# Kernel optimization log

Hardware: AMD Instinct MI355X
Metric: run time of the kernel (lower is better)

## Reference

```python
import jax, jax.numpy as jnp
import numpy as np

# --- static config (matches init_kwargs) ---
N = 10000          # nodes
E = 160000         # edges
MULT = 16          # multiplicity (in and out)
NL = 2             # number of irreps (lvals = [0, 1])
DIM = 4            # 1 + 3 spherical dims
EDGE_DIM = 32
HID = 128
RANK = 8           # low-rank radial weight rank
H = 4              # attention heads
HM = MULT // H     # head multiplicity
IDX = np.array([0, 1, 1, 1])  # irrep index for each of the DIM positions


def _radial(ef, w1, bb1, wl, bl, wr, br):
    """Low-rank radial weight: (E, edge_dim) -> (E, NL*MULT, NL*MULT)."""
    h = jax.nn.gelu(ef @ w1 + bb1, approximate=False)
    left = (h @ wl + bl).reshape(-1, NL * MULT, RANK)
    right = (h @ wr + br).reshape(-1, RANK, NL * MULT)
    return left @ right


def _conv(b1, b2, ef, f, src, w1, bb1, wl, bl, wr, br):
    """Equivariant convolution: gather -> basis contract -> radial bmm -> basis."""
    rw = _radial(ef, w1, bb1, wl, bl, wr, br)          # (E, 2*MULT, 2*MULT)
    f_src = f[src]                                      # (E, MULT, DIM)
    t = jnp.einsum('emd,edl->eml', f_src, b1)           # (E, MULT, NL)
    t = t.reshape(E, MULT * NL)                         # row-major, matches torch view
    t = jnp.einsum('erc,ec->er', rw, t)                 # (E, NL*MULT)
    t = t.reshape(E, MULT, NL)                          # (E, out_mult, nl2)
    return jnp.einsum('eml,eld->emd', t, b2)            # (E, MULT, DIM)


def reference(b1, b2, edge_feats, f, src_idx, dst_idx,
              q_w, q_b,
              k_w1, k_b1, k_wl, k_bl, k_wr, k_br,
              v_w1, v_b1, v_wl, v_bl, v_wr, v_br):
    # --- Q: equivariant linear on node features (per-irrep weights) ---
    W = q_w.reshape(NL, MULT, MULT)[IDX]                # (DIM, out_mult, in_mult)
    q = jnp.einsum('dom,nmd->nod', W, f)                # (N, MULT, DIM)
    q = q.at[:, :, 0].add(q_b[:, 0])                    # bias on scalar (l=0) slot

    # --- K, V: equivariant convolutions over edges ---
    k = _conv(b1, b2, edge_feats, f, src_idx, k_w1, k_b1, k_wl, k_bl, k_wr, k_br)
    v = _conv(b1, b2, edge_feats, f, src_idx, v_w1, v_b1, v_wl, v_bl, v_wr, v_br)

    # --- multi-head node_wise attention scores ---
    qh = q.reshape(N, H, HM * DIM)
    kh = k.reshape(E, H, HM * DIM)
    scale = jnp.sqrt(jnp.asarray(HM * DIM, q.dtype))
    scores = jnp.sum(qh[dst_idx] * kh, axis=-1) / scale  # (E, H)

    # --- segment softmax over edges grouped by destination node ---
    m = jax.ops.segment_max(scores, dst_idx, num_segments=N)       # (N, H)
    ex = jnp.exp(scores - m[dst_idx])
    den = jax.ops.segment_sum(ex, dst_idx, num_segments=N)         # (N, H)
    alpha = ex / jnp.maximum(den[dst_idx], 1e-9)                   # (E, H)

    # --- weighted scatter-reduce of values ---
    vh = v.reshape(E, H, HM * DIM)
    out = jax.ops.segment_sum(alpha[..., None] * vh, dst_idx, num_segments=N)
    return out.reshape(N, MULT, DIM)


def setup_inputs() -> dict:
    key = jax.random.key(0)
    ks = jax.random.split(key, 24)
    s = 0.05
    inp = {
        'b1': jax.random.normal(ks[0], (E, DIM, NL), jnp.float32),
        'b2': jax.random.normal(ks[1], (E, NL, DIM), jnp.float32),
        'edge_feats': jax.random.normal(ks[2], (E, EDGE_DIM), jnp.float32),
        'f': jax.random.normal(ks[3], (N, MULT, DIM), jnp.float32),
        'src_idx': jax.random.randint(ks[4], (E,), 0, N),
        'dst_idx': jax.random.randint(ks[5], (E,), 0, N),
        # Q equivariant linear
        'q_w': jax.random.normal(ks[6], (NL * MULT, MULT), jnp.float32) * s,
        'q_b': jnp.zeros((MULT, 1), jnp.float32),
    }
    for i, p in enumerate(['k', 'v']):
        base = 8 + i * 6
        inp[p + '_w1'] = jax.random.normal(ks[base + 0], (EDGE_DIM, HID), jnp.float32) * s
        inp[p + '_b1'] = jnp.zeros((HID,), jnp.float32)
        inp[p + '_wl'] = jax.random.normal(ks[base + 2], (HID, NL * MULT * RANK), jnp.float32) * s
        inp[p + '_bl'] = jnp.zeros((NL * MULT * RANK,), jnp.float32)
        inp[p + '_wr'] = jax.random.normal(ks[base + 4], (HID, RANK * NL * MULT), jnp.float32) * s
        inp[p + '_br'] = jnp.zeros((RANK * NL * MULT,), jnp.float32)
    return inp
```

## Files before the change

kernel.cpp:

```cpp
#include <hip/hip_runtime.h>
#include <hip/hip_bf16.h>
#include <math.h>

#define NNODES 10000
#define NEDGE  160000

typedef unsigned short u16;
using bf16x8 = __attribute__((ext_vector_type(8))) short;
using u16x8  = __attribute__((ext_vector_type(8))) unsigned short;
using f32x4  = __attribute__((ext_vector_type(4))) float;

static __device__ __forceinline__ u16 f2bf(float x) {
  unsigned u = __float_as_uint(x);
  u += 0x7FFFu + ((u >> 16) & 1u);
  return (u16)(u >> 16);
}
static __device__ __forceinline__ float bf2f(u16 h) {
  return __uint_as_float(((unsigned)h) << 16);
}
static __device__ __forceinline__ unsigned pack_bf16(float a, float b) {
  __hip_bfloat162 h = __float22bfloat162_rn(make_float2(a, b));
  return *(unsigned*)&h;
}
static __device__ __forceinline__ float fast_gelu(float x) {
  float y = x * __builtin_fmaf(0.07135481283f, x * x, 1.5957691216f);
  float e = __expf(y);
  return x - x * __builtin_amdgcn_rcpf(e + 1.0f);
}

__global__ void __launch_bounds__(1024) csr_build_kernel(
    const int* __restrict__ dst, int* __restrict__ rowptr, int* __restrict__ cursor) {
  __shared__ int hist[NNODES];
  __shared__ int part[1024];
  int t = threadIdx.x;
  for (int i = t; i < NNODES; i += 1024) hist[i] = 0;
  __syncthreads();
  const int4* d4 = (const int4*)dst;
  for (int i = t; i < NEDGE / 4; i += 1024) {
    int4 v = d4[i];
    atomicAdd(&hist[v.x], 1);
    atomicAdd(&hist[v.y], 1);
    atomicAdd(&hist[v.z], 1);
    atomicAdd(&hist[v.w], 1);
  }
  __syncthreads();
  int base = t * 10;
  int local[10];
  int s = 0;
#pragma unroll
  for (int i = 0; i < 10; ++i) {
    int idx = base + i;
    local[i] = (idx < NNODES) ? hist[idx] : 0;
    s += local[i];
  }
  part[t] = s;
  __syncthreads();
  for (int o = 1; o < 1024; o <<= 1) {
    int v = (t >= o) ? part[t - o] : 0;
    __syncthreads();
    part[t] += v;
    __syncthreads();
  }
  int run = (t == 0) ? 0 : part[t - 1];
#pragma unroll
  for (int i = 0; i < 10; ++i) {
    int idx = base + i;
    if (idx < NNODES) { rowptr[idx] = run; cursor[idx] = run; run += local[i]; }
  }
  if (t == 1023) rowptr[NNODES] = run;
}

__global__ void __launch_bounds__(256) setup_kernel(
    const float* __restrict__ kwr, const float* __restrict__ kwl,
    const float* __restrict__ vwr, const float* __restrict__ vwl,
    u16* __restrict__ Wsw,
    const float* __restrict__ kw1, const float* __restrict__ vw1,
    u16* __restrict__ W1sw,
    const float* __restrict__ f, const float* __restrict__ qw,
    const float* __restrict__ qb, float* __restrict__ q) {
  int b = blockIdx.x, tid = threadIdx.x;
  if (b < 512) {
    int idx = b * 256 + tid;
    int slot = idx >> 15;
    int w = idx & 32767;
    int j = w & 7, lane = (w >> 3) & 63, ks = (w >> 9) & 3, tg = w >> 11;
    int k   = ks * 32 + ((lane >> 4) << 3) + j;
    int col = (tg << 4) + (lane & 15);
    const float* s = (slot == 0) ? kwr : (slot == 1) ? kwl : (slot == 2) ? vwr : vwl;
    Wsw[idx] = f2bf(s[k * 256 + col]);
  } else if (b < 544) {
    int idx = (b - 512) * 256 + tid;
    int slot = idx >> 12;
    int w = idx & 4095;
    int j = w & 7, lane = (w >> 3) & 63, nt = w >> 9;
    int k   = ((lane >> 4) << 3) + j;
    int col = (nt << 4) + (lane & 15);
    const float* s = (slot == 0) ? kw1 : vw1;
    W1sw[idx] = f2bf(s[k * 128 + col]);
  } else {
    int i = (b - 544) * 256 + tid;
    if (i >= NNODES * 16) return;
    int n = i >> 4, o = i & 15;
    const float* frow = f + (size_t)n * 64;
    float o0 = 0.f, o1 = 0.f, o2 = 0.f, o3 = 0.f;
#pragma unroll
    for (int m = 0; m < 16; ++m) {
      float w0 = qw[o * 16 + m];
      float w1 = qw[(16 + o) * 16 + m];
      o0 += w0 * frow[m * 4 + 0];
      o1 += w1 * frow[m * 4 + 1];
      o2 += w1 * frow[m * 4 + 2];
      o3 += w1 * frow[m * 4 + 3];
    }
    o0 += qb[o];
    float4 r = make_float4(o0, o1, o2, o3);
    *(float4*)(q + (size_t)i * 4) = r;
  }
}

__global__ void __launch_bounds__(256) fill_t_kernel(
    const int* __restrict__ dst, const int* __restrict__ src,
    const float* __restrict__ f, const float* __restrict__ b1,
    const float* __restrict__ b2, const float* __restrict__ ef,
    int* __restrict__ cursor, char* __restrict__ comb) {
  int e = blockIdx.x * 256 + threadIdx.x;
  int n = dst[e];
  int pos = atomicAdd(&cursor[n], 1);
  char* rb = comb + (size_t)pos * 192;
  const float* frow = f + (size_t)src[e] * 64;
  const float* be = b1 + (size_t)e * 8;
  float b[8];
#pragma unroll
  for (int k = 0; k < 8; ++k) b[k] = be[k];
  uint4* tp = (uint4*)rb;
#pragma unroll
  for (int mh = 0; mh < 4; ++mh) {
    unsigned pk[4];
#pragma unroll
    for (int mi = 0; mi < 4; ++mi) {
      int m = mh * 4 + mi;
      float f0 = frow[m * 4 + 0], f1 = frow[m * 4 + 1], f2 = frow[m * 4 + 2], f3 = frow[m * 4 + 3];
      float t0 = f0 * b[0] + f1 * b[2] + f2 * b[4] + f3 * b[6];
      float t1 = f0 * b[1] + f1 * b[3] + f2 * b[5] + f3 * b[7];
      pk[mi] = pack_bf16(t0, t1);
    }
    tp[mh] = make_uint4(pk[0], pk[1], pk[2], pk[3]);
  }
  const float* efe = ef + (size_t)e * 32;
#pragma unroll
  for (int g = 0; g < 4; ++g) {
    float4 v0 = *(const float4*)&efe[g * 8];
    float4 v1 = *(const float4*)&efe[g * 8 + 4];
    tp[4 + g] = make_uint4(pack_bf16(v0.x, v0.y), pack_bf16(v0.z, v0.w),
                           pack_bf16(v1.x, v1.y), pack_bf16(v1.z, v1.w));
  }
  const float* b2e = b2 + (size_t)e * 8;
  *(float4*)(rb + 128) = *(const float4*)&b2e[0];
  *(float4*)(rb + 144) = *(const float4*)&b2e[4];
  *(int*)(rb + 160) = n;
}

__global__ void __launch_bounds__(512) conv_fused_kernel(
    const char* __restrict__ comb,
    const u16* __restrict__ w1sw_k, const float* __restrict__ b1h_k,
    const u16* __restrict__ wswr_k, const float* __restrict__ br_k,
    const u16* __restrict__ wswl_k, const float* __restrict__ bl_k,
    const u16* __restrict__ w1sw_v, const float* __restrict__ b1h_v,
    const u16* __restrict__ wswr_v, const float* __restrict__ br_v,
    const u16* __restrict__ wswl_v, const float* __restrict__ bl_v,
    const float* __restrict__ qbuf, float* __restrict__ exs,
    u16* __restrict__ kv) {
  __shared__ alignas(16) u16 sA[64 * 136];
  __shared__ alignas(16) u16 t_s[64 * 40];
  __shared__ alignas(16) float b2_s[64 * 12];
  __shared__ alignas(16) float u_s[64 * 12];
  __shared__ alignas(16) float t2_pool[64 * 36];
  float* t2_s = t2_pool;
  u16*   efs  = (u16*)t2_pool;

  int tid = threadIdx.x;
  int wave = tid >> 6, lane = tid & 63, quad = lane >> 4, l16 = lane & 15;
  bool kmode = (blockIdx.x & 1) == 0;
  size_t i0 = (size_t)(blockIdx.x >> 1) * 64;

  const u16*   w1sw = kmode ? w1sw_k : w1sw_v;
  const float* b1h  = kmode ? b1h_k  : b1h_v;
  const u16*   wsw_r = kmode ? wswr_k : wswr_v;
  const float* br    = kmode ? br_k   : br_v;
  const u16*   wsw_l = kmode ? wswl_k : wswl_v;
  const float* bl    = kmode ? bl_k   : bl_v;

  if (tid < 256) {
    int row = tid >> 2, seg = tid & 3;
    *(uint4*)&efs[row * 40 + seg * 8] =
        *(const uint4*)(comb + (i0 + row) * 192 + 64 + seg * 16);
    if (tid < 128) {
      int r2 = tid >> 1, half = tid & 1;
      *(float4*)&b2_s[r2 * 12 + half * 4] =
          *(const float4*)(comb + (i0 + r2) * 192 + 128 + half * 16);
    }
  } else {
    int j = tid - 256;
    int row = j >> 2, seg = j & 3;
    *(uint4*)&t_s[row * 40 + seg * 8] =
        *(const uint4*)(comb + (i0 + row) * 192 + seg * 16);
  }
  __syncthreads();

  {
    bf16x8 aw = *(const bf16x8*)&w1sw[(size_t)(wave * 64 + lane) * 8];
    float4 bias_h = *(const float4*)&b1h[wave * 16 + quad * 4];
#pragma unroll
    for (int nt = 0; nt < 4; ++nt) {
      bf16x8 be = *(const bf16x8*)&efs[(nt * 16 + l16) * 40 + quad * 8];
      f32x4 acch = __builtin_amdgcn_mfma_f32_16x16x32_bf16(aw, be, (f32x4){0.f, 0.f, 0.f, 0.f}, 0, 0, 0);
      unsigned p0 = pack_bf16(fast_gelu(acch[0] + bias_h.x), fast_gelu(acch[1] + bias_h.y));
      unsigned p1 = pack_bf16(fast_gelu(acch[2] + bias_h.z), fast_gelu(acch[3] + bias_h.w));
      *(uint2*)&sA[(nt * 16 + l16) * 136 + wave * 16 + quad * 4] = make_uint2(p0, p1);
    }
  }
  __syncthreads();

  f32x4 accr[2][4], accl[2][4];
#pragma unroll
  for (int mtl = 0; mtl < 2; ++mtl)
#pragma unroll
    for (int nt = 0; nt < 4; ++nt) {
      accr[mtl][nt] = (f32x4){0.f, 0.f, 0.f, 0.f};
      accl[mtl][nt] = (f32x4){0.f, 0.f, 0.f, 0.f};
    }
#pragma unroll
  for (int ks = 0; ks < 4; ++ks) {
    bf16x8 bfrag[4];
#pragma unroll
    for (int nt = 0; nt < 4; ++nt)
      bfrag[nt] = *(const bf16x8*)&sA[(nt * 16 + l16) * 136 + ks * 32 + quad * 8];
#pragma unroll
    for (int mtl = 0; mtl < 2; ++mtl) {
      int mtg = wave * 2 + mtl;
      bf16x8 ar = *(const bf16x8*)&wsw_r[(size_t)((mtg * 4 + ks) * 64 + lane) * 8];
      bf16x8 al = *(const bf16x8*)&wsw_l[(size_t)((mtg * 4 + ks) * 64 + lane) * 8];
#pragma unroll
      for (int nt = 0; nt < 4; ++nt) {
        accr[mtl][nt] = __builtin_amdgcn_mfma_f32_16x16x32_bf16(ar, bfrag[nt], accr[mtl][nt], 0, 0, 0);
        accl[mtl][nt] = __builtin_amdgcn_mfma_f32_16x16x32_bf16(al, bfrag[nt], accl[mtl][nt], 0, 0, 0);
      }
    }
  }

  float4 brv[2], blv[2];
#pragma unroll
  for (int mtl = 0; mtl < 2; ++mtl) {
    int colb = (wave * 2 + mtl) * 16 + quad * 4;
    brv[mtl] = *(const float4*)&br[colb];
    blv[mtl] = *(const float4*)&bl[colb];
  }

#pragma unroll
  for (int nt = 0; nt < 4; ++nt) {
    int e = nt * 16 + l16;
    ushort4 ta = *(const ushort4*)&t_s[e * 40 + 4 * quad];
    ushort4 tb = *(const ushort4*)&t_s[e * 40 + 16 + 4 * quad];
    float s = (accr[0][nt][0] + brv[0].x) * bf2f(ta.x)
            + (accr[0][nt][1] + brv[0].y) * bf2f(ta.y)
            + (accr[0][nt][2] + brv[0].z) * bf2f(ta.z)
            + (accr[0][nt][3] + brv[0].w) * bf2f(ta.w)
            + (accr[1][nt][0] + brv[1].x) * bf2f(tb.x)
            + (accr[1][nt][1] + brv[1].y) * bf2f(tb.y)
            + (accr[1][nt][2] + brv[1].z) * bf2f(tb.z)
            + (accr[1][nt][3] + brv[1].w) * bf2f(tb.w);
    s += __shfl_xor(s, 16);
    s += __shfl_xor(s, 32);
    if (quad == 0) u_s[e * 12 + wave] = s;
  }
  __syncthreads();

#pragma unroll
  for (int nt = 0; nt < 4; ++nt) {
    int e = nt * 16 + l16;
    float4 uv = *(const float4*)&u_s[e * 12 + 4 * (quad & 1)];
#pragma unroll
    for (int mtl = 0; mtl < 2; ++mtl) {
      float s = (accl[mtl][nt][0] + blv[mtl].x) * uv.x
              + (accl[mtl][nt][1] + blv[mtl].y) * uv.y
              + (accl[mtl][nt][2] + blv[mtl].z) * uv.z
              + (accl[mtl][nt][3] + blv[mtl].w) * uv.w;
      s += __shfl_xor(s, 16);
      if ((quad & 1) == 0)
        t2_s[e * 36 + 4 * wave + 2 * mtl + (quad >> 1)] = s;
    }
  }
  __syncthreads();

  {
    int e = tid >> 3, j = tid & 7;
    float4 t2 = *(const float4*)&t2_s[e * 36 + 4 * j];
    float4 b2a = *(const float4*)&b2_s[e * 12 + 0];
    float4 b2b = *(const float4*)&b2_s[e * 12 + 4];
    float v0 = t2.x * b2a.x + t2.y * b2b.x;
    float v1 = t2.x * b2a.y + t2.y * b2b.y;
    float v2 = t2.x * b2a.z + t2.y * b2b.z;
    float v3 = t2.x * b2a.w + t2.y * b2b.w;
    float v4 = t2.z * b2a.x + t2.w * b2b.x;
    float v5 = t2.z * b2a.y + t2.w * b2b.y;
    float v6 = t2.z * b2a.z + t2.w * b2b.z;
    float v7 = t2.z * b2a.w + t2.w * b2b.w;
    if (kmode) {
      int n = *(const int*)(comb + (i0 + e) * 192 + 160);
      const float* qr = qbuf + (size_t)n * 64 + j * 8;
      float4 qa = *(const float4*)&qr[0];
      float4 qc = *(const float4*)&qr[4];
      float s = v0 * qa.x + v1 * qa.y + v2 * qa.z + v3 * qa.w
              + v4 * qc.x + v5 * qc.y + v6 * qc.z + v7 * qc.w;
      s += __shfl_xor(s, 1);
      if ((j & 1) == 0)
        exs[(i0 + e) * 4 + (j >> 1)] = __expf(s * 0.25f);
    } else {
      unsigned q0 = pack_bf16(v0, v1);
      unsigned q1 = pack_bf16(v2, v3);
      unsigned q2 = pack_bf16(v4, v5);
      unsigned q3 = pack_bf16(v6, v7);
      *(uint4*)&kv[(i0 + e) * 64 + j * 8] = make_uint4(q0, q1, q2, q3);
    }
  }
}

__global__ void __launch_bounds__(256) attn_gather_kernel(
    const float* __restrict__ exs, const u16* __restrict__ kvv,
    const int* __restrict__ rowptr, float* __restrict__ outp) {
  int tid = threadIdx.x;
  int node = blockIdx.x * 4 + (tid >> 6);
  int lane = tid & 63, h = lane >> 4;
  int beg = rowptr[node], end = rowptr[node + 1];
  float num = 0.f, den = 0.f;
  int idx = beg;
  for (; idx + 2 <= end; idx += 2) {
    float e0 = exs[(size_t)idx * 4 + h];
    float e1 = exs[(size_t)(idx + 1) * 4 + h];
    float v0 = bf2f(kvv[(size_t)idx * 64 + lane]);
    float v1 = bf2f(kvv[(size_t)(idx + 1) * 64 + lane]);
    num += e0 * v0 + e1 * v1;
    den += e0 + e1;
  }
  if (idx < end) {
    float e0 = exs[(size_t)idx * 4 + h];
    num += e0 * bf2f(kvv[(size_t)idx * 64 + lane]);
    den += e0;
  }
  outp[(size_t)node * 64 + lane] = num / fmaxf(den, 1e-9f);
}

extern "C" void kernel_launch(void* const* d_in, const int* in_sizes, int n_in,
                              void* d_out, int out_size, void* d_ws, size_t ws_size,
                              hipStream_t stream) {
  const float* b1  = (const float*)d_in[0];
  const float* b2  = (const float*)d_in[1];
  const float* ef  = (const float*)d_in[2];
  const float* f   = (const float*)d_in[3];
  const int*   src = (const int*)d_in[4];
  const int*   dst = (const int*)d_in[5];
  const float* qw  = (const float*)d_in[6];
  const float* qb  = (const float*)d_in[7];
  const float* kw1 = (const float*)d_in[8];
  const float* kb1 = (const float*)d_in[9];
  const float* kwl = (const float*)d_in[10];
  const float* kbl = (const float*)d_in[11];
  const float* kwr = (const float*)d_in[12];
  const float* kbr = (const float*)d_in[13];
  const float* vw1 = (const float*)d_in[14];
  const float* vb1 = (const float*)d_in[15];
  const float* vwl = (const float*)d_in[16];
  const float* vbl = (const float*)d_in[17];
  const float* vwr = (const float*)d_in[18];
  const float* vbr = (const float*)d_in[19];
  float* outp = (float*)d_out;

  char* ws = (char*)d_ws;
  size_t off = 0;
  auto alloc = [&](size_t bytes) {
    char* p = ws + off;
    off += (bytes + 511) & ~(size_t)511;
    return p;
  };
  u16*   Wsw  = (u16*)  alloc((size_t)4 * 32768 * 2);
  u16*   W1sw = (u16*)  alloc((size_t)2 * 4096 * 2);
  char*  comb = (char*) alloc((size_t)NEDGE * 192);
  u16*   kvv  = (u16*)  alloc((size_t)NEDGE * 64 * 2);
  float* exb  = (float*)alloc((size_t)NEDGE * 4 * 4);
  float* qbuf = (float*)alloc((size_t)NNODES * 64 * 4);
  int*   rowptr = (int*)alloc((size_t)(NNODES + 1) * 4);
  int*   cursor = (int*)alloc((size_t)NNODES * 4);

  csr_build_kernel<<<1, 1024, 0, stream>>>(dst, rowptr, cursor);
  setup_kernel<<<1169, 256, 0, stream>>>(kwr, kwl, vwr, vwl, Wsw,
                                         kw1, vw1, W1sw,
                                         f, qw, qb, qbuf);
  fill_t_kernel<<<625, 256, 0, stream>>>(dst, src, f, b1, b2, ef,
                                         cursor, comb);

  conv_fused_kernel<<<5000, 512, 0, stream>>>(comb,
                                              W1sw + 0 * 4096, kb1,
                                              Wsw + 0 * 32768, kbr,
                                              Wsw + 1 * 32768, kbl,
                                              W1sw + 1 * 4096, vb1,
                                              Wsw + 2 * 32768, vbr,
                                              Wsw + 3 * 32768, vbl,
                                              qbuf, exb, kvv);

  attn_gather_kernel<<<2500, 256, 0, stream>>>(exb, kvv, rowptr, outp);
}
```

Baseline: 241.7 us.

## Replace CSR sort and gather with fused K/V conv and atomic scatter-add

Drops the single-block CSR build, the edge-permuting fill kernel and the per-node gather kernel. A single block now computes both K and V for 64 edges in original order: K first yields exp scores kept in shared memory, then V is scatter-added into per-node numerator and denominator buffers with float atomics. A small divide kernel normalises the result, and the setup kernel zeroes the accumulators. This removes the serial CSR build, the 192-byte-per-edge intermediate buffer and the kv/exs round trips. In exchange it adds heavy global atomic traffic, nine atomics per thread, and the summation order becomes nondeterministic.

```diff
diff --git a/kernel.cpp b/kernel.cpp
--- a/kernel.cpp
+++ b/kernel.cpp
@@ -7,7 +7,6 @@
 
 typedef unsigned short u16;
 using bf16x8 = __attribute__((ext_vector_type(8))) short;
-using u16x8  = __attribute__((ext_vector_type(8))) unsigned short;
 using f32x4  = __attribute__((ext_vector_type(4))) float;
 
 static __device__ __forceinline__ u16 f2bf(float x) {
@@ -26,48 +25,6 @@
   float y = x * __builtin_fmaf(0.07135481283f, x * x, 1.5957691216f);
   float e = __expf(y);
   return x - x * __builtin_amdgcn_rcpf(e + 1.0f);
-}
-
-__global__ void __launch_bounds__(1024) csr_build_kernel(
-    const int* __restrict__ dst, int* __restrict__ rowptr, int* __restrict__ cursor) {
-  __shared__ int hist[NNODES];
-  __shared__ int part[1024];
-  int t = threadIdx.x;
-  for (int i = t; i < NNODES; i += 1024) hist[i] = 0;
-  __syncthreads();
-  const int4* d4 = (const int4*)dst;
-  for (int i = t; i < NEDGE / 4; i += 1024) {
-    int4 v = d4[i];
-    atomicAdd(&hist[v.x], 1);
-    atomicAdd(&hist[v.y], 1);
-    atomicAdd(&hist[v.z], 1);
-    atomicAdd(&hist[v.w], 1);
-  }
-  __syncthreads();
-  int base = t * 10;
-  int local[10];
-  int s = 0;
-#pragma unroll
-  for (int i = 0; i < 10; ++i) {
-    int idx = base + i;
-    local[i] = (idx < NNODES) ? hist[idx] : 0;
-    s += local[i];
-  }
-  part[t] = s;
-  __syncthreads();
-  for (int o = 1; o < 1024; o <<= 1) {
-    int v = (t >= o) ? part[t - o] : 0;
-    __syncthreads();
-    part[t] += v;
-    __syncthreads();
-  }
-  int run = (t == 0) ? 0 : part[t - 1];
-#pragma unroll
-  for (int i = 0; i < 10; ++i) {
-    int idx = base + i;
-    if (idx < NNODES) { rowptr[idx] = run; cursor[idx] = run; run += local[i]; }
-  }
-  if (t == 1023) rowptr[NNODES] = run;
 }
 
 __global__ void __launch_bounds__(256) setup_kernel(
@@ -77,7 +34,8 @@
     const float* __restrict__ kw1, const float* __restrict__ vw1,
     u16* __restrict__ W1sw,
     const float* __restrict__ f, const float* __restrict__ qw,
-    const float* __restrict__ qb, float* __restrict__ q) {
+    const float* __restrict__ qb, float* __restrict__ q,
+    float* __restrict__ zbase) {
   int b = blockIdx.x, tid = threadIdx.x;
   if (b < 512) {
     int idx = b * 256 + tid;
@@ -97,7 +55,7 @@
     int col = (nt << 4) + (lane & 15);
     const float* s = (slot == 0) ? kw1 : vw1;
     W1sw[idx] = f2bf(s[k * 128 + col]);
-  } else {
+  } else if (b < 1169) {
     int i = (b - 544) * 256 + tid;
     if (i >= NNODES * 16) return;
     int n = i >> 4, o = i & 15;
@@ -115,239 +73,215 @@
     o0 += qb[o];
     float4 r = make_float4(o0, o1, o2, o3);
     *(float4*)(q + (size_t)i * 4) = r;
+  } else {
+    int idx = (b - 1169) * 256 + tid;
+    if (idx < 170000)
+      *(float4*)((char*)zbase + (size_t)idx * 16) = make_float4(0.f, 0.f, 0.f, 0.f);
   }
 }
 
-__global__ void __launch_bounds__(256) fill_t_kernel(
-    const int* __restrict__ dst, const int* __restrict__ src,
-    const float* __restrict__ f, const float* __restrict__ b1,
-    const float* __restrict__ b2, const float* __restrict__ ef,
-    int* __restrict__ cursor, char* __restrict__ comb) {
-  int e = blockIdx.x * 256 + threadIdx.x;
-  int n = dst[e];
-  int pos = atomicAdd(&cursor[n], 1);
-  char* rb = comb + (size_t)pos * 192;
-  const float* frow = f + (size_t)src[e] * 64;
-  const float* be = b1 + (size_t)e * 8;
-  float b[8];
-#pragma unroll
-  for (int k = 0; k < 8; ++k) b[k] = be[k];
-  uint4* tp = (uint4*)rb;
-#pragma unroll
-  for (int mh = 0; mh < 4; ++mh) {
-    unsigned pk[4];
-#pragma unroll
-    for (int mi = 0; mi < 4; ++mi) {
-      int m = mh * 4 + mi;
-      float f0 = frow[m * 4 + 0], f1 = frow[m * 4 + 1], f2 = frow[m * 4 + 2], f3 = frow[m * 4 + 3];
-      float t0 = f0 * b[0] + f1 * b[2] + f2 * b[4] + f3 * b[6];
-      float t1 = f0 * b[1] + f1 * b[3] + f2 * b[5] + f3 * b[7];
-      pk[mi] = pack_bf16(t0, t1);
-    }
-    tp[mh] = make_uint4(pk[0], pk[1], pk[2], pk[3]);
-  }
-  const float* efe = ef + (size_t)e * 32;
-#pragma unroll
-  for (int g = 0; g < 4; ++g) {
-    float4 v0 = *(const float4*)&efe[g * 8];
-    float4 v1 = *(const float4*)&efe[g * 8 + 4];
-    tp[4 + g] = make_uint4(pack_bf16(v0.x, v0.y), pack_bf16(v0.z, v0.w),
-                           pack_bf16(v1.x, v1.y), pack_bf16(v1.z, v1.w));
-  }
-  const float* b2e = b2 + (size_t)e * 8;
-  *(float4*)(rb + 128) = *(const float4*)&b2e[0];
-  *(float4*)(rb + 144) = *(const float4*)&b2e[4];
-  *(int*)(rb + 160) = n;
-}
-
-__global__ void __launch_bounds__(512) conv_fused_kernel(
-    const char* __restrict__ comb,
+__global__ void __launch_bounds__(512) convkv_kernel(
+    const float* __restrict__ ef, const float* __restrict__ f,
+    const float* __restrict__ b1, const float* __restrict__ b2,
+    const int* __restrict__ src, const int* __restrict__ dst,
     const u16* __restrict__ w1sw_k, const float* __restrict__ b1h_k,
     const u16* __restrict__ wswr_k, const float* __restrict__ br_k,
     const u16* __restrict__ wswl_k, const float* __restrict__ bl_k,
     const u16* __restrict__ w1sw_v, const float* __restrict__ b1h_v,
     const u16* __restrict__ wswr_v, const float* __restrict__ br_v,
     const u16* __restrict__ wswl_v, const float* __restrict__ bl_v,
-    const float* __restrict__ qbuf, float* __restrict__ exs,
-    u16* __restrict__ kv) {
+    const float* __restrict__ qbuf, float* __restrict__ num,
+    float* __restrict__ den) {
   __shared__ alignas(16) u16 sA[64 * 136];
   __shared__ alignas(16) u16 t_s[64 * 40];
   __shared__ alignas(16) float b2_s[64 * 12];
   __shared__ alignas(16) float u_s[64 * 12];
   __shared__ alignas(16) float t2_pool[64 * 36];
+  __shared__ float exs_s[64 * 4];
+  __shared__ int   nn[64];
   float* t2_s = t2_pool;
   u16*   efs  = (u16*)t2_pool;
 
   int tid = threadIdx.x;
   int wave = tid >> 6, lane = tid & 63, quad = lane >> 4, l16 = lane & 15;
-  bool kmode = (blockIdx.x & 1) == 0;
-  size_t i0 = (size_t)(blockIdx.x >> 1) * 64;
-
-  const u16*   w1sw = kmode ? w1sw_k : w1sw_v;
-  const float* b1h  = kmode ? b1h_k  : b1h_v;
-  const u16*   wsw_r = kmode ? wswr_k : wswr_v;
-  const float* br    = kmode ? br_k   : br_v;
-  const u16*   wsw_l = kmode ? wswl_k : wswl_v;
-  const float* bl    = kmode ? bl_k   : bl_v;
-
-  if (tid < 256) {
-    int row = tid >> 2, seg = tid & 3;
-    *(uint4*)&efs[row * 40 + seg * 8] =
-        *(const uint4*)(comb + (i0 + row) * 192 + 64 + seg * 16);
-    if (tid < 128) {
-      int r2 = tid >> 1, half = tid & 1;
-      *(float4*)&b2_s[r2 * 12 + half * 4] =
-          *(const float4*)(comb + (i0 + r2) * 192 + 128 + half * 16);
-    }
-  } else {
-    int j = tid - 256;
-    int row = j >> 2, seg = j & 3;
-    *(uint4*)&t_s[row * 40 + seg * 8] =
-        *(const uint4*)(comb + (i0 + row) * 192 + seg * 16);
+  size_t i0 = (size_t)blockIdx.x * 64;
+  int e8 = tid >> 3, j8 = tid & 7;
+
+  {
+    float4 ev = *(const float4*)&ef[(i0 + e8) * 32 + j8 * 4];
+    *(uint2*)&efs[e8 * 40 + j8 * 4] =
+        make_uint2(pack_bf16(ev.x, ev.y), pack_bf16(ev.z, ev.w));
+    int se = src[i0 + e8];
+    const float* frow = f + (size_t)se * 64;
+    const float* be = b1 + (i0 + e8) * 8;
+    float bb[8];
+#pragma unroll
+    for (int k = 0; k < 8; ++k) bb[k] = be[k];
+    float4 a = *(const float4*)&frow[(2 * j8) * 4];
+    float t0 = a.x * bb[0] + a.y * bb[2] + a.z * bb[4] + a.w * bb[6];
+    float t1 = a.x * bb[1] + a.y * bb[3] + a.z * bb[5] + a.w * bb[7];
+    float4 c = *(const float4*)&frow[(2 * j8 + 1) * 4];
+    float t2a = c.x * bb[0] + c.y * bb[2] + c.z * bb[4] + c.w * bb[6];
+    float t3a = c.x * bb[1] + c.y * bb[3] + c.z * bb[5] + c.w * bb[7];
+    *(uint2*)&t_s[e8 * 40 + j8 * 4] =
+        make_uint2(pack_bf16(t0, t1), pack_bf16(t2a, t3a));
+    b2_s[e8 * 12 + j8] = b2[(i0 + e8) * 8 + j8];
+    if (tid < 64) nn[tid] = dst[i0 + tid];
   }
   __syncthreads();
 
-  {
-    bf16x8 aw = *(const bf16x8*)&w1sw[(size_t)(wave * 64 + lane) * 8];
-    float4 bias_h = *(const float4*)&b1h[wave * 16 + quad * 4];
+#pragma unroll 1
+  for (int ph = 0; ph < 2; ++ph) {
+    const u16*   w1sw  = ph ? w1sw_v : w1sw_k;
+    const float* b1h   = ph ? b1h_v  : b1h_k;
+    const u16*   wsw_r = ph ? wswr_v : wswr_k;
+    const float* br    = ph ? br_v   : br_k;
+    const u16*   wsw_l = ph ? wswl_v : wswl_k;
+    const float* bl    = ph ? bl_v   : bl_k;
+
+    if (ph == 1) {
+      __syncthreads();
+      float4 ev = *(const float4*)&ef[(i0 + e8) * 32 + j8 * 4];
+      *(uint2*)&efs[e8 * 40 + j8 * 4] =
+          make_uint2(pack_bf16(ev.x, ev.y), pack_bf16(ev.z, ev.w));
+      __syncthreads();
+    }
+
+    {
+      bf16x8 aw = *(const bf16x8*)&w1sw[(size_t)(wave * 64 + lane) * 8];
+      float4 bias_h = *(const float4*)&b1h[wave * 16 + quad * 4];
+#pragma unroll
+      for (int nt = 0; nt < 4; ++nt) {
+        bf16x8 bef = *(const bf16x8*)&efs[(nt * 16 + l16) * 40 + quad * 8];
+        f32x4 acch = __builtin_amdgcn_mfma_f32_16x16x32_bf16(aw, bef, (f32x4){0.f, 0.f, 0.f, 0.f}, 0, 0, 0);
+        unsigned p0 = pack_bf16(fast_gelu(acch[0] + bias_h.x), fast_gelu(acch[1] + bias_h.y));
+        unsigned p1 = pack_bf16(fast_gelu(acch[2] + bias_h.z), fast_gelu(acch[3] + bias_h.w));
+        *(uint2*)&sA[(nt * 16 + l16) * 136 + wave * 16 + quad * 4] = make_uint2(p0, p1);
+      }
+    }
+    __syncthreads();
+
+    f32x4 accr[2][4], accl[2][4];
+#pragma unroll
+    for (int mtl = 0; mtl < 2; ++mtl)
+#pragma unroll
+      for (int nt = 0; nt < 4; ++nt) {
+        accr[mtl][nt] = (f32x4){0.f, 0.f, 0.f, 0.f};
+        accl[mtl][nt] = (f32x4){0.f, 0.f, 0.f, 0.f};
+      }
+#pragma unroll
+    for (int ks = 0; ks < 4; ++ks) {
+      bf16x8 bfrag[4];
+#pragma unroll
+      for (int nt = 0; nt < 4; ++nt)
+        bfrag[nt] = *(const bf16x8*)&sA[(nt * 16 + l16) * 136 + ks * 32 + quad * 8];
+#pragma unroll
+      for (int mtl = 0; mtl < 2; ++mtl) {
+        int mtg = wave * 2 + mtl;
+        bf16x8 ar = *(const bf16x8*)&wsw_r[(size_t)((mtg * 4 + ks) * 64 + lane) * 8];
+        bf16x8 al = *(const bf16x8*)&wsw_l[(size_t)((mtg * 4 + ks) * 64 + lane) * 8];
+#pragma unroll
+        for (int nt = 0; nt < 4; ++nt) {
+          accr[mtl][nt] = __builtin_amdgcn_mfma_f32_16x16x32_bf16(ar, bfrag[nt], accr[mtl][nt], 0, 0, 0);
+          accl[mtl][nt] = __builtin_amdgcn_mfma_f32_16x16x32_bf16(al, bfrag[nt], accl[mtl][nt], 0, 0, 0);
+        }
+      }
+    }
+
+    float4 brv[2], blv[2];
+#pragma unroll
+    for (int mtl = 0; mtl < 2; ++mtl) {
+      int colb = (wave * 2 + mtl) * 16 + quad * 4;
+      brv[mtl] = *(const float4*)&br[colb];
+      blv[mtl] = *(const float4*)&bl[colb];
+    }
+
 #pragma unroll
     for (int nt = 0; nt < 4; ++nt) {
-      bf16x8 be = *(const bf16x8*)&efs[(nt * 16 + l16) * 40 + quad * 8];
-      f32x4 acch = __builtin_amdgcn_mfma_f32_16x16x32_bf16(aw, be, (f32x4){0.f, 0.f, 0.f, 0.f}, 0, 0, 0);
-      unsigned p0 = pack_bf16(fast_gelu(acch[0] + bias_h.x), fast_gelu(acch[1] + bias_h.y));
-      unsigned p1 = pack_bf16(fast_gelu(acch[2] + bias_h.z), fast_gelu(acch[3] + bias_h.w));
-      *(uint2*)&sA[(nt * 16 + l16) * 136 + wave * 16 + quad * 4] = make_uint2(p0, p1);
+      int e = nt * 16 + l16;
+      ushort4 ta = *(const ushort4*)&t_s[e * 40 + 4 * quad];
+      ushort4 tb = *(const ushort4*)&t_s[e * 40 + 16 + 4 * quad];
+      float s = (accr[0][nt][0] + brv[0].x) * bf2f(ta.x)
+              + (accr[0][nt][1] + brv[0].y) * bf2f(ta.y)
+              + (accr[0][nt][2] + brv[0].z) * bf2f(ta.z)
+              + (accr[0][nt][3] + brv[0].w) * bf2f(ta.w)
+              + (accr[1][nt][0] + brv[1].x) * bf2f(tb.x)
+              + (accr[1][nt][1] + brv[1].y) * bf2f(tb.y)
+              + (accr[1][nt][2] + brv[1].z) * bf2f(tb.z)
+              + (accr[1][nt][3] + brv[1].w) * bf2f(tb.w);
+      s += __shfl_xor(s, 16);
+      s += __shfl_xor(s, 32);
+      if (quad == 0) u_s[e * 12 + wave] = s;
+    }
+    __syncthreads();
+
+#pragma unroll
+    for (int nt = 0; nt < 4; ++nt) {
+      int e = nt * 16 + l16;
+      float4 uv = *(const float4*)&u_s[e * 12 + 4 * (quad & 1)];
+#pragma unroll
+      for (int mtl = 0; mtl < 2; ++mtl) {
+        float s = (accl[mtl][nt][0] + blv[mtl].x) * uv.x
+                + (accl[mtl][nt][1] + blv[mtl].y) * uv.y
+                + (accl[mtl][nt][2] + blv[mtl].z) * uv.z
+                + (accl[mtl][nt][3] + blv[mtl].w) * uv.w;
+        s += __shfl_xor(s, 16);
+        if ((quad & 1) == 0)
+          t2_s[e * 36 + 4 * wave + 2 * mtl + (quad >> 1)] = s;
+      }
+    }
+    __syncthreads();
+
+    {
+      float4 t2 = *(const float4*)&t2_s[e8 * 36 + 4 * j8];
+      float4 b2a = *(const float4*)&b2_s[e8 * 12 + 0];
+      float4 b2b = *(const float4*)&b2_s[e8 * 12 + 4];
+      float v0 = t2.x * b2a.x + t2.y * b2b.x;
+      float v1 = t2.x * b2a.y + t2.y * b2b.y;
+      float v2 = t2.x * b2a.z + t2.y * b2b.z;
+      float v3 = t2.x * b2a.w + t2.y * b2b.w;
+      float v4 = t2.z * b2a.x + t2.w * b2b.x;
+      float v5 = t2.z * b2a.y + t2.w * b2b.y;
+      float v6 = t2.z * b2a.z + t2.w * b2b.z;
+      float v7 = t2.z * b2a.w + t2.w * b2b.w;
+      int n = nn[e8];
+      if (ph == 0) {
+        const float* qr = qbuf + (size_t)n * 64 + j8 * 8;
+        float4 qa = *(const float4*)&qr[0];
+        float4 qc = *(const float4*)&qr[4];
+        float s = v0 * qa.x + v1 * qa.y + v2 * qa.z + v3 * qa.w
+                + v4 * qc.x + v5 * qc.y + v6 * qc.z + v7 * qc.w;
+        s += __shfl_xor(s, 1);
+        if ((j8 & 1) == 0)
+          exs_s[e8 * 4 + (j8 >> 1)] = __expf(s * 0.25f);
+      } else {
+        float ex = exs_s[e8 * 4 + (j8 >> 1)];
+        float* np = num + (size_t)n * 64 + j8 * 8;
+        atomicAdd(&np[0], ex * v0);
+        atomicAdd(&np[1], ex * v1);
+        atomicAdd(&np[2], ex * v2);
+        atomicAdd(&np[3], ex * v3);
+        atomicAdd(&np[4], ex * v4);
+        atomicAdd(&np[5], ex * v5);
+        atomicAdd(&np[6], ex * v6);
+        atomicAdd(&np[7], ex * v7);
+        if ((j8 & 1) == 0)
+          atomicAdd(&den[n * 4 + (j8 >> 1)], ex);
+      }
     }
   }
-  __syncthreads();
-
-  f32x4 accr[2][4], accl[2][4];
-#pragma unroll
-  for (int mtl = 0; mtl < 2; ++mtl)
-#pragma unroll
-    for (int nt = 0; nt < 4; ++nt) {
-      accr[mtl][nt] = (f32x4){0.f, 0.f, 0.f, 0.f};
-      accl[mtl][nt] = (f32x4){0.f, 0.f, 0.f, 0.f};
-    }
-#pragma unroll
-  for (int ks = 0; ks < 4; ++ks) {
-    bf16x8 bfrag[4];
-#pragma unroll
-    for (int nt = 0; nt < 4; ++nt)
-      bfrag[nt] = *(const bf16x8*)&sA[(nt * 16 + l16) * 136 + ks * 32 + quad * 8];
-#pragma unroll
-    for (int mtl = 0; mtl < 2; ++mtl) {
-      int mtg = wave * 2 + mtl;
-      bf16x8 ar = *(const bf16x8*)&wsw_r[(size_t)((mtg * 4 + ks) * 64 + lane) * 8];
-      bf16x8 al = *(const bf16x8*)&wsw_l[(size_t)((mtg * 4 + ks) * 64 + lane) * 8];
-#pragma unroll
-      for (int nt = 0; nt < 4; ++nt) {
-        accr[mtl][nt] = __builtin_amdgcn_mfma_f32_16x16x32_bf16(ar, bfrag[nt], accr[mtl][nt], 0, 0, 0);
-        accl[mtl][nt] = __builtin_amdgcn_mfma_f32_16x16x32_bf16(al, bfrag[nt], accl[mtl][nt], 0, 0, 0);
-      }
-    }
-  }
-
-  float4 brv[2], blv[2];
-#pragma unroll
-  for (int mtl = 0; mtl < 2; ++mtl) {
-    int colb = (wave * 2 + mtl) * 16 + quad * 4;
-    brv[mtl] = *(const float4*)&br[colb];
-    blv[mtl] = *(const float4*)&bl[colb];
-  }
-
-#pragma unroll
-  for (int nt = 0; nt < 4; ++nt) {
-    int e = nt * 16 + l16;
-    ushort4 ta = *(const ushort4*)&t_s[e * 40 + 4 * quad];
-    ushort4 tb = *(const ushort4*)&t_s[e * 40 + 16 + 4 * quad];
-    float s = (accr[0][nt][0] + brv[0].x) * bf2f(ta.x)
-            + (accr[0][nt][1] + brv[0].y) * bf2f(ta.y)
-            + (accr[0][nt][2] + brv[0].z) * bf2f(ta.z)
-            + (accr[0][nt][3] + brv[0].w) * bf2f(ta.w)
-            + (accr[1][nt][0] + brv[1].x) * bf2f(tb.x)
-            + (accr[1][nt][1] + brv[1].y) * bf2f(tb.y)
-            + (accr[1][nt][2] + brv[1].z) * bf2f(tb.z)
-            + (accr[1][nt][3] + brv[1].w) * bf2f(tb.w);
-    s += __shfl_xor(s, 16);
-    s += __shfl_xor(s, 32);
-    if (quad == 0) u_s[e * 12 + wave] = s;
-  }
-  __syncthreads();
-
-#pragma unroll
-  for (int nt = 0; nt < 4; ++nt) {
-    int e = nt * 16 + l16;
-    float4 uv = *(const float4*)&u_s[e * 12 + 4 * (quad & 1)];
-#pragma unroll
-    for (int mtl = 0; mtl < 2; ++mtl) {
-      float s = (accl[mtl][nt][0] + blv[mtl].x) * uv.x
-              + (accl[mtl][nt][1] + blv[mtl].y) * uv.y
-              + (accl[mtl][nt][2] + blv[mtl].z) * uv.z
-              + (accl[mtl][nt][3] + blv[mtl].w) * uv.w;
-      s += __shfl_xor(s, 16);
-      if ((quad & 1) == 0)
-        t2_s[e * 36 + 4 * wave + 2 * mtl + (quad >> 1)] = s;
-    }
-  }
-  __syncthreads();
-
-  {
-    int e = tid >> 3, j = tid & 7;
-    float4 t2 = *(const float4*)&t2_s[e * 36 + 4 * j];
-    float4 b2a = *(const float4*)&b2_s[e * 12 + 0];
-    float4 b2b = *(const float4*)&b2_s[e * 12 + 4];
-    float v0 = t2.x * b2a.x + t2.y * b2b.x;
-    float v1 = t2.x * b2a.y + t2.y * b2b.y;
-    float v2 = t2.x * b2a.z + t2.y * b2b.z;
-    float v3 = t2.x * b2a.w + t2.y * b2b.w;
-    float v4 = t2.z * b2a.x + t2.w * b2b.x;
-    float v5 = t2.z * b2a.y + t2.w * b2b.y;
-    float v6 = t2.z * b2a.z + t2.w * b2b.z;
-    float v7 = t2.z * b2a.w + t2.w * b2b.w;
-    if (kmode) {
-      int n = *(const int*)(comb + (i0 + e) * 192 + 160);
-      const float* qr = qbuf + (size_t)n * 64 + j * 8;
-      float4 qa = *(const float4*)&qr[0];
-      float4 qc = *(const float4*)&qr[4];
-      float s = v0 * qa.x + v1 * qa.y + v2 * qa.z + v3 * qa.w
-              + v4 * qc.x + v5 * qc.y + v6 * qc.z + v7 * qc.w;
-      s += __shfl_xor(s, 1);
-      if ((j & 1) == 0)
-        exs[(i0 + e) * 4 + (j >> 1)] = __expf(s * 0.25f);
-    } else {
-      unsigned q0 = pack_bf16(v0, v1);
-      unsigned q1 = pack_bf16(v2, v3);
-      unsigned q2 = pack_bf16(v4, v5);
-      unsigned q3 = pack_bf16(v6, v7);
-      *(uint4*)&kv[(i0 + e) * 64 + j * 8] = make_uint4(q0, q1, q2, q3);
-    }
-  }
-}
-
-__global__ void __launch_bounds__(256) attn_gather_kernel(
-    const float* __restrict__ exs, const u16* __restrict__ kvv,
-    const int* __restrict__ rowptr, float* __restrict__ outp) {
-  int tid = threadIdx.x;
-  int node = blockIdx.x * 4 + (tid >> 6);
-  int lane = tid & 63, h = lane >> 4;
-  int beg = rowptr[node], end = rowptr[node + 1];
-  float num = 0.f, den = 0.f;
-  int idx = beg;
-  for (; idx + 2 <= end; idx += 2) {
-    float e0 = exs[(size_t)idx * 4 + h];
-    float e1 = exs[(size_t)(idx + 1) * 4 + h];
-    float v0 = bf2f(kvv[(size_t)idx * 64 + lane]);
-    float v1 = bf2f(kvv[(size_t)(idx + 1) * 64 + lane]);
-    num += e0 * v0 + e1 * v1;
-    den += e0 + e1;
-  }
-  if (idx < end) {
-    float e0 = exs[(size_t)idx * 4 + h];
-    num += e0 * bf2f(kvv[(size_t)idx * 64 + lane]);
-    den += e0;
-  }
-  outp[(size_t)node * 64 + lane] = num / fmaxf(den, 1e-9f);
+}
+
+__global__ void __launch_bounds__(256) divide_kernel(
+    const float* __restrict__ num, const float* __restrict__ den,
+    float* __restrict__ outp) {
+  int idx = blockIdx.x * 256 + threadIdx.x;
+  int n = idx >> 4, g = idx & 15;
+  float d = den[n * 4 + (g >> 2)];
+  float r = 1.0f / fmaxf(d, 1e-9f);
+  float4 v = *(const float4*)&num[(size_t)idx * 4];
+  float4 o = make_float4(v.x * r, v.y * r, v.z * r, v.w * r);
+  *(float4*)&outp[(size_t)idx * 4] = o;
 }
 
 extern "C" void kernel_launch(void* const* d_in, const int* in_sizes, int n_in,
@@ -384,28 +318,22 @@
   };
   u16*   Wsw  = (u16*)  alloc((size_t)4 * 32768 * 2);
   u16*   W1sw = (u16*)  alloc((size_t)2 * 4096 * 2);
-  char*  comb = (char*) alloc((size_t)NEDGE * 192);
-  u16*   kvv  = (u16*)  alloc((size_t)NEDGE * 64 * 2);
-  float* exb  = (float*)alloc((size_t)NEDGE * 4 * 4);
   float* qbuf = (float*)alloc((size_t)NNODES * 64 * 4);
-  int*   rowptr = (int*)alloc((size_t)(NNODES + 1) * 4);
-  int*   cursor = (int*)alloc((size_t)NNODES * 4);
-
-  csr_build_kernel<<<1, 1024, 0, stream>>>(dst, rowptr, cursor);
-  setup_kernel<<<1169, 256, 0, stream>>>(kwr, kwl, vwr, vwl, Wsw,
+  float* numb = (float*)alloc((size_t)NNODES * 64 * 4);
+  float* denb = (float*)alloc((size_t)NNODES * 4 * 4);
+
+  setup_kernel<<<1834, 256, 0, stream>>>(kwr, kwl, vwr, vwl, Wsw,
                                          kw1, vw1, W1sw,
-                                         f, qw, qb, qbuf);
-  fill_t_kernel<<<625, 256, 0, stream>>>(dst, src, f, b1, b2, ef,
-                                         cursor, comb);
-
-  conv_fused_kernel<<<5000, 512, 0, stream>>>(comb,
-                                              W1sw + 0 * 4096, kb1,
-                                              Wsw + 0 * 32768, kbr,
-                                              Wsw + 1 * 32768, kbl,
-                                              W1sw + 1 * 4096, vb1,
-                                              Wsw + 2 * 32768, vbr,
-                                              Wsw + 3 * 32768, vbl,
-                                              qbuf, exb, kvv);
-
-  attn_gather_kernel<<<2500, 256, 0, stream>>>(exb, kvv, rowptr, outp);
-}
+                                         f, qw, qb, qbuf, numb);
+
+  convkv_kernel<<<2500, 512, 0, stream>>>(ef, f, b1, b2, src, dst,
+                                          W1sw + 0 * 4096, kb1,
+                                          Wsw + 0 * 32768, kbr,
+                                          Wsw + 1 * 32768, kbl,
+                                          W1sw + 1 * 4096, vb1,
+                                          Wsw + 2 * 32768, vbr,
+                                          Wsw + 3 * 32768, vbl,
+                                          qbuf, numb, denb);
+
+  divide_kernel<<<625, 256, 0, stream>>>(numb, denb, outp);
+}
```

Result: slower. 435.0 us (+80.0%).

## Parallelize CSR histogram across grid via global atomics folded into setup kernel

Applied to the files above, without the earlier changes.

Replaces the single-block CSR build, which had one block histogram all 160k destination indices in shared memory, with a grid-wide global-atomic histogram. The histogram now runs as extra blocks of the setup kernel, followed by a separate single-block scan kernel. The goal is to take a serial one-block bottleneck off the critical path. In exchange it adds a memset and an extra kernel launch, and uses contended global atomics instead of LDS atomics.

```diff
diff --git a/kernel.cpp b/kernel.cpp
--- a/kernel.cpp
+++ b/kernel.cpp
@@ -7,7 +7,6 @@
 
 typedef unsigned short u16;
 using bf16x8 = __attribute__((ext_vector_type(8))) short;
-using u16x8  = __attribute__((ext_vector_type(8))) unsigned short;
 using f32x4  = __attribute__((ext_vector_type(4))) float;
 
 static __device__ __forceinline__ u16 f2bf(float x) {
@@ -26,48 +25,6 @@
   float y = x * __builtin_fmaf(0.07135481283f, x * x, 1.5957691216f);
   float e = __expf(y);
   return x - x * __builtin_amdgcn_rcpf(e + 1.0f);
-}
-
-__global__ void __launch_bounds__(1024) csr_build_kernel(
-    const int* __restrict__ dst, int* __restrict__ rowptr, int* __restrict__ cursor) {
-  __shared__ int hist[NNODES];
-  __shared__ int part[1024];
-  int t = threadIdx.x;
-  for (int i = t; i < NNODES; i += 1024) hist[i] = 0;
-  __syncthreads();
-  const int4* d4 = (const int4*)dst;
-  for (int i = t; i < NEDGE / 4; i += 1024) {
-    int4 v = d4[i];
-    atomicAdd(&hist[v.x], 1);
-    atomicAdd(&hist[v.y], 1);
-    atomicAdd(&hist[v.z], 1);
-    atomicAdd(&hist[v.w], 1);
-  }
-  __syncthreads();
-  int base = t * 10;
-  int local[10];
-  int s = 0;
-#pragma unroll
-  for (int i = 0; i < 10; ++i) {
-    int idx = base + i;
-    local[i] = (idx < NNODES) ? hist[idx] : 0;
-    s += local[i];
-  }
-  part[t] = s;
-  __syncthreads();
-  for (int o = 1; o < 1024; o <<= 1) {
-    int v = (t >= o) ? part[t - o] : 0;
-    __syncthreads();
-    part[t] += v;
-    __syncthreads();
-  }
-  int run = (t == 0) ? 0 : part[t - 1];
-#pragma unroll
-  for (int i = 0; i < 10; ++i) {
-    int idx = base + i;
-    if (idx < NNODES) { rowptr[idx] = run; cursor[idx] = run; run += local[i]; }
-  }
-  if (t == 1023) rowptr[NNODES] = run;
 }
 
 __global__ void __launch_bounds__(256) setup_kernel(
@@ -77,7 +34,8 @@
     const float* __restrict__ kw1, const float* __restrict__ vw1,
     u16* __restrict__ W1sw,
     const float* __restrict__ f, const float* __restrict__ qw,
-    const float* __restrict__ qb, float* __restrict__ q) {
+    const float* __restrict__ qb, float* __restrict__ q,
+    const int* __restrict__ dst, int* __restrict__ cursor) {
   int b = blockIdx.x, tid = threadIdx.x;
   if (b < 512) {
     int idx = b * 256 + tid;
@@ -97,7 +55,7 @@
     int col = (nt << 4) + (lane & 15);
     const float* s = (slot == 0) ? kw1 : vw1;
     W1sw[idx] = f2bf(s[k * 128 + col]);
-  } else {
+  } else if (b < 1169) {
     int i = (b - 544) * 256 + tid;
     if (i >= NNODES * 16) return;
     int n = i >> 4, o = i & 15;
@@ -115,7 +73,40 @@
     o0 += qb[o];
     float4 r = make_float4(o0, o1, o2, o3);
     *(float4*)(q + (size_t)i * 4) = r;
-  }
+  } else {
+    int e = (b - 1169) * 256 + tid;
+    atomicAdd(&cursor[dst[e]], 1);
+  }
+}
+
+__global__ void __launch_bounds__(1024) scan_kernel(
+    int* __restrict__ cursor, int* __restrict__ rowptr) {
+  __shared__ int part[1024];
+  int t = threadIdx.x;
+  int base = t * 10;
+  int local[10];
+  int s = 0;
+#pragma unroll
+  for (int i = 0; i < 10; ++i) {
+    int idx = base + i;
+    local[i] = (idx < NNODES) ? cursor[idx] : 0;
+    s += local[i];
+  }
+  part[t] = s;
+  __syncthreads();
+  for (int o = 1; o < 1024; o <<= 1) {
+    int v = (t >= o) ? part[t - o] : 0;
+    __syncthreads();
+    part[t] += v;
+    __syncthreads();
+  }
+  int run = (t == 0) ? 0 : part[t - 1];
+#pragma unroll
+  for (int i = 0; i < 10; ++i) {
+    int idx = base + i;
+    if (idx < NNODES) { rowptr[idx] = run; cursor[idx] = run; run += local[i]; }
+  }
+  if (t == 1023) rowptr[NNODES] = run;
 }
 
 __global__ void __launch_bounds__(256) fill_t_kernel(
@@ -391,10 +382,12 @@
   int*   rowptr = (int*)alloc((size_t)(NNODES + 1) * 4);
   int*   cursor = (int*)alloc((size_t)NNODES * 4);
 
-  csr_build_kernel<<<1, 1024, 0, stream>>>(dst, rowptr, cursor);
-  setup_kernel<<<1169, 256, 0, stream>>>(kwr, kwl, vwr, vwl, Wsw,
+  hipMemsetAsync(cursor, 0, (size_t)NNODES * 4, stream);
+  setup_kernel<<<1794, 256, 0, stream>>>(kwr, kwl, vwr, vwl, Wsw,
                                          kw1, vw1, W1sw,
-                                         f, qw, qb, qbuf);
+                                         f, qw, qb, qbuf,
+                                         dst, cursor);
+  scan_kernel<<<1, 1024, 0, stream>>>(cursor, rowptr);
   fill_t_kernel<<<625, 256, 0, stream>>>(dst, src, f, b1, b2, ef,
                                          cursor, comb);
 
```

Measured after the change: 242.3 us. Within noise of the previous version (+0.3%).
